# Performance work log

Measured on AMD Instinct MI355X. Metric: run time of the kernel, lower is better.

## Reference

```python
import jax, jax.numpy as jnp
import numpy as np

N, E = 20000, 320000
IN, HID, OUT, H = 128, 32, 1, 4
EPS = 1e-16  # PyG softmax epsilon


def _p(key, shape, scale=0.05):
    return jax.random.normal(key, shape, dtype=jnp.float32) * scale


def setup_inputs() -> dict:
    key = jax.random.key(0)
    ks = jax.random.split(key, 20)
    d = {
        "x": jax.random.normal(ks[0], (N, IN), dtype=jnp.float32),
        "edge_src": jax.random.randint(ks[1], (E,), 0, N, dtype=jnp.int32),
        "edge_dst": jax.random.randint(ks[2], (E,), 0, N, dtype=jnp.int32),
        # layer 1: TransformerConv(IN, HID, H)  ->  [N, H*HID]
        "W1q": _p(ks[3], (IN, H * HID)), "b1q": jnp.zeros((H * HID,), jnp.float32),
        "W1k": _p(ks[4], (IN, H * HID)), "b1k": jnp.zeros((H * HID,), jnp.float32),
        "W1v": _p(ks[5], (IN, H * HID)), "b1v": jnp.zeros((H * HID,), jnp.float32),
        "W1s": _p(ks[6], (IN, H * HID)), "b1s": jnp.zeros((H * HID,), jnp.float32),
        # layer 2: TransformerConv(H*HID, OUT, H) -> [N, H*OUT]
        "W2q": _p(ks[7], (H * HID, H * OUT)), "b2q": jnp.zeros((H * OUT,), jnp.float32),
        "W2k": _p(ks[8], (H * HID, H * OUT)), "b2k": jnp.zeros((H * OUT,), jnp.float32),
        "W2v": _p(ks[9], (H * HID, H * OUT)), "b2v": jnp.zeros((H * OUT,), jnp.float32),
        "W2s": _p(ks[10], (H * HID, H * OUT)), "b2s": jnp.zeros((H * OUT,), jnp.float32),
        # final nn.Linear(heads, 1)
        "Wl": _p(ks[11], (H, 1)), "bl": jnp.zeros((1,), jnp.float32),
    }
    return d


def transformer_conv(x, src, dst, Wq, bq, Wk, bk, Wv, bv, Ws, bs, heads, ch):
    n = x.shape[0]
    q = (x @ Wq + bq).reshape(n, heads, ch)
    k = (x @ Wk + bk).reshape(n, heads, ch)
    v = (x @ Wv + bv).reshape(n, heads, ch)
    qi, kj, vj = q[dst], k[src], v[src]            # [E,H,C] gathers
    score = (qi * kj).sum(-1) / jnp.sqrt(jnp.float32(ch))  # [E,H]
    m = jax.ops.segment_max(score, dst, num_segments=n)    # segment softmax by target
    e = jnp.exp(score - m[dst])
    s = jax.ops.segment_sum(e, dst, num_segments=n)
    alpha = e / (s[dst] + EPS)                              # [E,H]
    agg = jax.ops.segment_sum(alpha[:, :, None] * vj, dst, num_segments=n)  # [N,H,C]
    return agg.reshape(n, heads * ch) + x @ Ws + bs          # concat + root skip


def reference(x, edge_src, edge_dst,
              W1q, b1q, W1k, b1k, W1v, b1v, W1s, b1s,
              W2q, b2q, W2k, b2k, W2v, b2v, W2s, b2s,
              Wl, bl):
    h = transformer_conv(x, edge_src, edge_dst, W1q, b1q, W1k, b1k, W1v, b1v, W1s, b1s, H, HID)
    h = jax.nn.relu(h)  # dropout is identity in eval
    h = transformer_conv(h, edge_src, edge_dst, W2q, b2q, W2k, b2k, W2v, b2v, W2s, b2s, H, OUT)
    y = h @ Wl + bl                      # [N,1]
    return y.mean(axis=0, keepdims=True)  # [1,1]
```

## Files before the change

kernel.cpp:

```cpp
#include <hip/hip_runtime.h>
#include <math.h>

static constexpr float EPS_PYG = 1e-16f;
static constexpr float INV_SQRT32 = 0.17677669529663687f;

typedef short bf16x8 __attribute__((ext_vector_type(8)));
typedef float f32x4 __attribute__((ext_vector_type(4)));

__device__ inline unsigned short f2bf(float f) {
    union { float f; unsigned u; } x; x.f = f;
    unsigned r = x.u + 0x7FFFu + ((x.u >> 16) & 1u);
    return (unsigned short)(r >> 16);
}
__device__ inline float bf_hi(unsigned u) {
    union { unsigned u; float f; } x; x.u = u & 0xFFFF0000u; return x.f;
}
__device__ inline float bf_lo(unsigned u) {
    union { unsigned u; float f; } x; x.u = u << 16; return x.f;
}

__global__ void deg_kernel(const int* __restrict__ dst, int* __restrict__ deg, int E) {
    int e = blockIdx.x * blockDim.x + threadIdx.x;
    if (e < E) atomicAdd(&deg[dst[e]], 1);
}

__global__ __launch_bounds__(1024) void scan_kernel(const int* __restrict__ deg,
                                                    int* __restrict__ row_off, int n) {
    const int t = threadIdx.x;
    const int CH = (n + 1023) >> 10;
    const int base = t * CH;
    int vals[32];
    int sum = 0;
#pragma unroll 4
    for (int i = 0; i < CH; ++i) {
        int idx = base + i;
        int v = (idx < n) ? deg[idx] : 0;
        sum += v;
        vals[i] = sum;
    }
    const int lane = t & 63;
    const int wid = t >> 6;
    int wsum = sum;
#pragma unroll
    for (int off = 1; off < 64; off <<= 1) {
        int o = __shfl_up(wsum, off, 64);
        if (lane >= off) wsum += o;
    }
    __shared__ int wtot[16];
    if (lane == 63) wtot[wid] = wsum;
    __syncthreads();
    if (t < 64) {
        int v = (t < 16) ? wtot[t] : 0;
        int inc = v;
#pragma unroll
        for (int off = 1; off < 16; off <<= 1) {
            int o = __shfl_up(inc, off, 64);
            if (t >= off) inc += o;
        }
        if (t < 16) wtot[t] = inc - v;
    }
    __syncthreads();
    const int toff = wtot[wid] + (wsum - sum);
    if (t == 0) row_off[0] = 0;
#pragma unroll 4
    for (int i = 0; i < CH; ++i) {
        int idx = base + i;
        if (idx < n) row_off[idx + 1] = toff + vals[i];
    }
}

__global__ void scatter_kernel(const int* __restrict__ src, const int* __restrict__ dst,
                               const int* __restrict__ row_off, int* __restrict__ cursor,
                               int* __restrict__ csr_src, int E) {
    int e = blockIdx.x * blockDim.x + threadIdx.x;
    if (e < E) {
        int d = dst[e];
        int pos = row_off[d] + atomicAdd(&cursor[d], 1);
        csr_src[pos] = src[e];
    }
}

__global__ __launch_bounds__(256) void prep_kernel(
    const float4* __restrict__ X, ushort4* __restrict__ Xb, int total4,
    const float* __restrict__ Wq, const float* __restrict__ Wk,
    const float* __restrict__ Wv, const float* __restrict__ Wsk,
    unsigned short* __restrict__ Wbt)
{
    const int b = blockIdx.x;
    if (b < 4) {
        const float* W = (b == 0) ? Wq : (b == 1) ? Wk : (b == 2) ? Wv : Wsk;
        for (int i = threadIdx.x; i < 16384; i += 256) {
            int k = i >> 7, nn = i & 127;
            Wbt[b * 16384 + nn * 128 + k] = f2bf(W[i]);
        }
    } else {
        int i = (b - 4) * 256 + threadIdx.x;
        if (i < total4) {
            float4 v = X[i];
            ushort4 o;
            o.x = f2bf(v.x); o.y = f2bf(v.y); o.z = f2bf(v.z); o.w = f2bf(v.w);
            Xb[i] = o;
        }
    }
}

__global__ __launch_bounds__(256) void gemm1_mfma(
    const unsigned short* __restrict__ Xb, const unsigned short* __restrict__ Wbt,
    const float* __restrict__ bq, const float* __restrict__ bk,
    const float* __restrict__ bv, const float* __restrict__ bsk,
    float* __restrict__ Q, unsigned int* __restrict__ KV,
    float* __restrict__ S, int n)
{
    const int mat = blockIdx.y;
    const unsigned short* W = Wbt + (size_t)mat * 16384;
    const float* bias = (mat == 0) ? bq : (mat == 1) ? bk : (mat == 2) ? bv : bsk;

    const int tid  = threadIdx.x;
    const int wave = tid >> 6;
    const int lane = tid & 63;
    const int m    = lane & 15;
    const int quad = lane >> 4;
    const int r0   = blockIdx.x * 64 + wave * 16;

    int arow = r0 + m;
    if (arow >= n) arow = n - 1;

    f32x4 acc[8] = {};
#pragma unroll
    for (int kc = 0; kc < 128; kc += 32) {
        bf16x8 a = *(const bf16x8*)(Xb + (size_t)arow * 128 + kc + quad * 8);
#pragma unroll
        for (int ct = 0; ct < 8; ++ct) {
            bf16x8 bfr = *(const bf16x8*)(W + (ct * 16 + m) * 128 + kc + quad * 8);
            acc[ct] = __builtin_amdgcn_mfma_f32_16x16x32_bf16(a, bfr, acc[ct], 0, 0, 0);
        }
    }

#pragma unroll
    for (int ct = 0; ct < 8; ++ct) {
        const int col = ct * 16 + m;
        const float bb = bias[col];
#pragma unroll
        for (int r = 0; r < 4; ++r) {
            const int row = r0 + quad * 4 + r;
            if (row < n) {
                float val = acc[ct][r] + bb;
                size_t idx = (size_t)row * 128 + col;
                if (mat == 0)      Q[idx] = val;
                else if (mat == 3) S[idx] = val;
                else ((unsigned short*)KV)[idx * 2 + ((mat == 1) ? 1 : 0)] = f2bf(val);
            }
        }
    }
}

__global__ __launch_bounds__(128) void l1_agg_kernel(
    const float* __restrict__ Q, const unsigned int* __restrict__ KV,
    const float* __restrict__ S,
    const int* __restrict__ row_off, const int* __restrict__ csr_src,
    float* __restrict__ H1, int n)
{
    const int node = blockIdx.x;
    const int t = threadIdx.x;
    const float q = Q[(size_t)node * 128 + t];
    const int beg = row_off[node], end = row_off[node + 1];

    float l = 0.f, acc = 0.f;
    int pos = beg;
    for (; pos + 4 <= end; pos += 4) {
        int s0 = csr_src[pos];
        int s1 = csr_src[pos + 1];
        int s2 = csr_src[pos + 2];
        int s3 = csr_src[pos + 3];
        unsigned u0 = KV[(size_t)s0 * 128 + t];
        unsigned u1 = KV[(size_t)s1 * 128 + t];
        unsigned u2 = KV[(size_t)s2 * 128 + t];
        unsigned u3 = KV[(size_t)s3 * 128 + t];
        float p0 = q * bf_hi(u0), p1 = q * bf_hi(u1);
        float p2 = q * bf_hi(u2), p3 = q * bf_hi(u3);
        p0 += __shfl_xor(p0, 16, 32); p1 += __shfl_xor(p1, 16, 32);
        p2 += __shfl_xor(p2, 16, 32); p3 += __shfl_xor(p3, 16, 32);
        p0 += __shfl_xor(p0, 8, 32);  p1 += __shfl_xor(p1, 8, 32);
        p2 += __shfl_xor(p2, 8, 32);  p3 += __shfl_xor(p3, 8, 32);
        p0 += __shfl_xor(p0, 4, 32);  p1 += __shfl_xor(p1, 4, 32);
        p2 += __shfl_xor(p2, 4, 32);  p3 += __shfl_xor(p3, 4, 32);
        p0 += __shfl_xor(p0, 2, 32);  p1 += __shfl_xor(p1, 2, 32);
        p2 += __shfl_xor(p2, 2, 32);  p3 += __shfl_xor(p3, 2, 32);
        p0 += __shfl_xor(p0, 1, 32);  p1 += __shfl_xor(p1, 1, 32);
        p2 += __shfl_xor(p2, 1, 32);  p3 += __shfl_xor(p3, 1, 32);
        float e0 = __expf(p0 * INV_SQRT32);
        float e1 = __expf(p1 * INV_SQRT32);
        float e2 = __expf(p2 * INV_SQRT32);
        float e3 = __expf(p3 * INV_SQRT32);
        l   += (e0 + e1) + (e2 + e3);
        acc += (e0 * bf_lo(u0) + e1 * bf_lo(u1)) + (e2 * bf_lo(u2) + e3 * bf_lo(u3));
    }
    for (; pos < end; ++pos) {
        int s0 = csr_src[pos];
        unsigned u0 = KV[(size_t)s0 * 128 + t];
        float p0 = q * bf_hi(u0);
        p0 += __shfl_xor(p0, 16, 32);
        p0 += __shfl_xor(p0, 8, 32);
        p0 += __shfl_xor(p0, 4, 32);
        p0 += __shfl_xor(p0, 2, 32);
        p0 += __shfl_xor(p0, 1, 32);
        float e0 = __expf(p0 * INV_SQRT32);
        l += e0;
        acc += e0 * bf_lo(u0);
    }
    float out = acc / (l + EPS_PYG) + S[(size_t)node * 128 + t];
    H1[(size_t)node * 128 + t] = fmaxf(out, 0.f);
}

__global__ __launch_bounds__(256) void gemm2_kernel(
    const float* __restrict__ H1,
    const float* __restrict__ Wq, const float* __restrict__ Wk,
    const float* __restrict__ Wv, const float* __restrict__ Wsk,
    const float* __restrict__ bq, const float* __restrict__ bk,
    const float* __restrict__ bv, const float* __restrict__ bsk,
    float4* __restrict__ Q2, float4* __restrict__ K2,
    float4* __restrict__ V2, float4* __restrict__ S2, int n)
{
    __shared__ float Hs[64][129];
    __shared__ float Wt[128][16];
    __shared__ float bt[16];

    const int tid = threadIdx.x;
    const int r0 = blockIdx.x * 64;

    for (int i = tid; i < 2048; i += 256) {
        int row = i >> 4, col = i & 15;
        int mt = col >> 2, c = col & 3;
        const float* Wm = (mt == 0) ? Wq : (mt == 1) ? Wk : (mt == 2) ? Wv : Wsk;
        Wt[row][col] = Wm[row * 4 + c];
    }
    if (tid < 16) {
        int mt = tid >> 2;
        const float* bm = (mt == 0) ? bq : (mt == 1) ? bk : (mt == 2) ? bv : bsk;
        bt[tid] = bm[tid & 3];
    }
    for (int f = tid; f < 2048; f += 256) {
        int row = f >> 5, c4 = f & 31;
        float4 val = make_float4(0.f, 0.f, 0.f, 0.f);
        if (r0 + row < n) val = ((const float4*)H1)[(size_t)(r0 + row) * 32 + c4];
        Hs[row][c4 * 4 + 0] = val.x;
        Hs[row][c4 * 4 + 1] = val.y;
        Hs[row][c4 * 4 + 2] = val.z;
        Hs[row][c4 * 4 + 3] = val.w;
    }
    __syncthreads();

    const int nl = tid & 63;
    const int jg = tid >> 6;
    float a0 = 0.f, a1 = 0.f, a2 = 0.f, a3 = 0.f;
#pragma unroll 4
    for (int k = 0; k < 128; ++k) {
        float h = Hs[nl][k];
        a0 += h * Wt[k][jg * 4 + 0];
        a1 += h * Wt[k][jg * 4 + 1];
        a2 += h * Wt[k][jg * 4 + 2];
        a3 += h * Wt[k][jg * 4 + 3];
    }
    int node = r0 + nl;
    if (node < n) {
        float4 o = make_float4(a0 + bt[jg * 4 + 0], a1 + bt[jg * 4 + 1],
                               a2 + bt[jg * 4 + 2], a3 + bt[jg * 4 + 3]);
        float4* Cm = (jg == 0) ? Q2 : (jg == 1) ? K2 : (jg == 2) ? V2 : S2;
        Cm[node] = o;
    }
}

__global__ void init_out_kernel(float* __restrict__ out, const float* __restrict__ bl) {
    out[0] = bl[0];
}

__global__ __launch_bounds__(256) void l2_agg_kernel(
    const float4* __restrict__ Q2, const float4* __restrict__ K2,
    const float4* __restrict__ V2, const float4* __restrict__ S2,
    const int* __restrict__ row_off, const int* __restrict__ csr_src,
    const float* __restrict__ Wl, float* __restrict__ out, int n, float invn)
{
    const int nd = blockIdx.x * 256 + threadIdx.x;
    float y = 0.f;
    if (nd < n) {
        float4 q = Q2[nd];
        float l0 = 0.f, l1 = 0.f, l2 = 0.f, l3 = 0.f;
        float a0 = 0.f, a1 = 0.f, a2 = 0.f, a3 = 0.f;
        const int beg = row_off[nd], end = row_off[nd + 1];
        for (int pos = beg; pos < end; ++pos) {
            int src = csr_src[pos];
            float4 k = K2[src];
            float4 v = V2[src];
            float e0 = __expf(q.x * k.x);
            float e1 = __expf(q.y * k.y);
            float e2 = __expf(q.z * k.z);
            float e3 = __expf(q.w * k.w);
            l0 += e0; a0 += e0 * v.x;
            l1 += e1; a1 += e1 * v.y;
            l2 += e2; a2 += e2 * v.z;
            l3 += e3; a3 += e3 * v.w;
        }
        float4 sk = S2[nd];
        float h0 = a0 / (l0 + EPS_PYG) + sk.x;
        float h1 = a1 / (l1 + EPS_PYG) + sk.y;
        float h2 = a2 / (l2 + EPS_PYG) + sk.z;
        float h3 = a3 / (l3 + EPS_PYG) + sk.w;
        y = (h0 * Wl[0] + h1 * Wl[1] + h2 * Wl[2] + h3 * Wl[3]) * invn;
    }
    __shared__ float red[256];
    red[threadIdx.x] = y;
    __syncthreads();
    for (int off = 128; off > 0; off >>= 1) {
        if (threadIdx.x < (unsigned)off) red[threadIdx.x] += red[threadIdx.x + off];
        __syncthreads();
    }
    if (threadIdx.x == 0) atomicAdd(out, red[0]);
}

extern "C" void kernel_launch(void* const* d_in, const int* in_sizes, int n_in,
                              void* d_out, int out_size, void* d_ws, size_t ws_size,
                              hipStream_t stream) {
    const float* x        = (const float*)d_in[0];
    const int*   edge_src = (const int*)d_in[1];
    const int*   edge_dst = (const int*)d_in[2];
    const float* W1q = (const float*)d_in[3];  const float* b1q = (const float*)d_in[4];
    const float* W1k = (const float*)d_in[5];  const float* b1k = (const float*)d_in[6];
    const float* W1v = (const float*)d_in[7];  const float* b1v = (const float*)d_in[8];
    const float* W1s = (const float*)d_in[9];  const float* b1s = (const float*)d_in[10];
    const float* W2q = (const float*)d_in[11]; const float* b2q = (const float*)d_in[12];
    const float* W2k = (const float*)d_in[13]; const float* b2k = (const float*)d_in[14];
    const float* W2v = (const float*)d_in[15]; const float* b2v = (const float*)d_in[16];
    const float* W2s = (const float*)d_in[17]; const float* b2s = (const float*)d_in[18];
    const float* Wl  = (const float*)d_in[19]; const float* bl  = (const float*)d_in[20];

    const int N = in_sizes[0] / 128;
    const int E = in_sizes[1];
    float* out = (float*)d_out;

    float* ws  = (float*)d_ws;
    size_t off = 0;
    float*        Q1  = ws + off; off += (size_t)N * 128;
    unsigned int* KV  = (unsigned int*)(ws + off); off += (size_t)N * 128;
    float*        S1  = ws + off; off += (size_t)N * 128;
    float*        H1  = ws + off; off += (size_t)N * 128;
    float*        q2  = ws + off; off += (size_t)N * 4;
    float*        k2  = ws + off; off += (size_t)N * 4;
    float*        v2  = ws + off; off += (size_t)N * 4;
    float*        s2  = ws + off; off += (size_t)N * 4;
    unsigned short* Xb  = (unsigned short*)(ws + off); off += (size_t)N * 64;
    unsigned short* Wbt = (unsigned short*)(ws + off); off += 4 * 16384 / 2;
    int* ibase   = (int*)(ws + off);
    int* deg     = ibase;
    int* cursor  = ibase + N;
    int* row_off = ibase + 2 * N;
    int* csr_src = ibase + 3 * N + 1;

    hipMemsetAsync(deg, 0, (size_t)2 * N * sizeof(int), stream);
    deg_kernel<<<(E + 255) / 256, 256, 0, stream>>>(edge_dst, deg, E);
    scan_kernel<<<1, 1024, 0, stream>>>(deg, row_off, N);
    scatter_kernel<<<(E + 255) / 256, 256, 0, stream>>>(edge_src, edge_dst, row_off,
                                                        cursor, csr_src, E);

    const int total4 = N * 32;
    prep_kernel<<<4 + (total4 + 255) / 256, 256, 0, stream>>>(
        (const float4*)x, (ushort4*)Xb, total4, W1q, W1k, W1v, W1s, Wbt);

    {
        dim3 grid((N + 63) / 64, 4);
        gemm1_mfma<<<grid, 256, 0, stream>>>(Xb, Wbt, b1q, b1k, b1v, b1s,
                                             Q1, KV, S1, N);
    }
    l1_agg_kernel<<<N, 128, 0, stream>>>(Q1, KV, S1, row_off, csr_src, H1, N);

    gemm2_kernel<<<(N + 63) / 64, 256, 0, stream>>>(H1, W2q, W2k, W2v, W2s,
                                                    b2q, b2k, b2v, b2s,
                                                    (float4*)q2, (float4*)k2,
                                                    (float4*)v2, (float4*)s2, N);
    init_out_kernel<<<1, 1, 0, stream>>>(out, bl);
    l2_agg_kernel<<<(N + 255) / 256, 256, 0, stream>>>((const float4*)q2, (const float4*)k2,
                                                       (const float4*)v2, (const float4*)s2,
                                                       row_off, csr_src, Wl, out, N,
                                                       1.0f / (float)N);
}
```

Baseline: 258.1 us.

## Record atomic slots in degree pass, fuse K/V gemm, interleave layer-2 K/V

The degree pass now saves each edge's atomic slot, so the scatter pass computes its CSR position without a second atomic pass or a cursor memset. The layer-1 K and V projections are computed in the same block, sharing the A-operand loads and writing packed bf16 pairs as one 32-bit store instead of two strided half-word stores. Layer-2 K and V are interleaved so each edge gather reads adjacent data, and the out-init kernel is folded into the scan kernel. The cost is an extra E-sized slot buffer and more registers in the fused K/V gemm path.

```diff
diff --git a/kernel.cpp b/kernel.cpp
--- a/kernel.cpp
+++ b/kernel.cpp
@@ -19,13 +19,16 @@
     union { unsigned u; float f; } x; x.u = u << 16; return x.f;
 }
 
-__global__ void deg_kernel(const int* __restrict__ dst, int* __restrict__ deg, int E) {
+__global__ void deg_slot_kernel(const int* __restrict__ dst, int* __restrict__ deg,
+                                int* __restrict__ slot, int E) {
     int e = blockIdx.x * blockDim.x + threadIdx.x;
-    if (e < E) atomicAdd(&deg[dst[e]], 1);
+    if (e < E) slot[e] = atomicAdd(&deg[dst[e]], 1);
 }
 
 __global__ __launch_bounds__(1024) void scan_kernel(const int* __restrict__ deg,
-                                                    int* __restrict__ row_off, int n) {
+                                                    int* __restrict__ row_off, int n,
+                                                    float* __restrict__ out,
+                                                    const float* __restrict__ bl) {
     const int t = threadIdx.x;
     const int CH = (n + 1023) >> 10;
     const int base = t * CH;
@@ -61,7 +64,7 @@
     }
     __syncthreads();
     const int toff = wtot[wid] + (wsum - sum);
-    if (t == 0) row_off[0] = 0;
+    if (t == 0) { row_off[0] = 0; out[0] = bl[0]; }
 #pragma unroll 4
     for (int i = 0; i < CH; ++i) {
         int idx = base + i;
@@ -70,14 +73,10 @@
 }
 
 __global__ void scatter_kernel(const int* __restrict__ src, const int* __restrict__ dst,
-                               const int* __restrict__ row_off, int* __restrict__ cursor,
+                               const int* __restrict__ row_off, const int* __restrict__ slot,
                                int* __restrict__ csr_src, int E) {
     int e = blockIdx.x * blockDim.x + threadIdx.x;
-    if (e < E) {
-        int d = dst[e];
-        int pos = row_off[d] + atomicAdd(&cursor[d], 1);
-        csr_src[pos] = src[e];
-    }
+    if (e < E) csr_src[row_off[dst[e]] + slot[e]] = src[e];
 }
 
 __global__ __launch_bounds__(256) void prep_kernel(
@@ -111,9 +110,7 @@
     float* __restrict__ Q, unsigned int* __restrict__ KV,
     float* __restrict__ S, int n)
 {
-    const int mat = blockIdx.y;
-    const unsigned short* W = Wbt + (size_t)mat * 16384;
-    const float* bias = (mat == 0) ? bq : (mat == 1) ? bk : (mat == 2) ? bv : bsk;
+    const int mode = blockIdx.y;
 
     const int tid  = threadIdx.x;
     const int wave = tid >> 6;
@@ -125,30 +122,59 @@
     int arow = r0 + m;
     if (arow >= n) arow = n - 1;
 
-    f32x4 acc[8] = {};
-#pragma unroll
-    for (int kc = 0; kc < 128; kc += 32) {
-        bf16x8 a = *(const bf16x8*)(Xb + (size_t)arow * 128 + kc + quad * 8);
+    if (mode == 1) {
+        const unsigned short* WK = Wbt + 16384;
+        const unsigned short* WV = Wbt + 2 * 16384;
+        f32x4 accK[8] = {};
+        f32x4 accV[8] = {};
+#pragma unroll
+        for (int kc = 0; kc < 128; kc += 32) {
+            bf16x8 a = *(const bf16x8*)(Xb + (size_t)arow * 128 + kc + quad * 8);
+#pragma unroll
+            for (int ct = 0; ct < 8; ++ct) {
+                bf16x8 bk8 = *(const bf16x8*)(WK + (ct * 16 + m) * 128 + kc + quad * 8);
+                accK[ct] = __builtin_amdgcn_mfma_f32_16x16x32_bf16(a, bk8, accK[ct], 0, 0, 0);
+                bf16x8 bv8 = *(const bf16x8*)(WV + (ct * 16 + m) * 128 + kc + quad * 8);
+                accV[ct] = __builtin_amdgcn_mfma_f32_16x16x32_bf16(a, bv8, accV[ct], 0, 0, 0);
+            }
+        }
 #pragma unroll
         for (int ct = 0; ct < 8; ++ct) {
-            bf16x8 bfr = *(const bf16x8*)(W + (ct * 16 + m) * 128 + kc + quad * 8);
-            acc[ct] = __builtin_amdgcn_mfma_f32_16x16x32_bf16(a, bfr, acc[ct], 0, 0, 0);
-        }
-    }
-
-#pragma unroll
-    for (int ct = 0; ct < 8; ++ct) {
-        const int col = ct * 16 + m;
-        const float bb = bias[col];
-#pragma unroll
-        for (int r = 0; r < 4; ++r) {
-            const int row = r0 + quad * 4 + r;
-            if (row < n) {
-                float val = acc[ct][r] + bb;
-                size_t idx = (size_t)row * 128 + col;
-                if (mat == 0)      Q[idx] = val;
-                else if (mat == 3) S[idx] = val;
-                else ((unsigned short*)KV)[idx * 2 + ((mat == 1) ? 1 : 0)] = f2bf(val);
+            const int col = ct * 16 + m;
+            const float bbk = bk[col], bbv = bv[col];
+#pragma unroll
+            for (int r = 0; r < 4; ++r) {
+                const int row = r0 + quad * 4 + r;
+                if (row < n) {
+                    unsigned kb = f2bf(accK[ct][r] + bbk);
+                    unsigned vb = f2bf(accV[ct][r] + bbv);
+                    KV[(size_t)row * 128 + col] = (kb << 16) | vb;
+                }
+            }
+        }
+    } else {
+        const int mat = (mode == 0) ? 0 : 3;
+        const unsigned short* W = Wbt + (size_t)mat * 16384;
+        const float* bias = (mode == 0) ? bq : bsk;
+        float* C = (mode == 0) ? Q : S;
+        f32x4 acc[8] = {};
+#pragma unroll
+        for (int kc = 0; kc < 128; kc += 32) {
+            bf16x8 a = *(const bf16x8*)(Xb + (size_t)arow * 128 + kc + quad * 8);
+#pragma unroll
+            for (int ct = 0; ct < 8; ++ct) {
+                bf16x8 bfr = *(const bf16x8*)(W + (ct * 16 + m) * 128 + kc + quad * 8);
+                acc[ct] = __builtin_amdgcn_mfma_f32_16x16x32_bf16(a, bfr, acc[ct], 0, 0, 0);
+            }
+        }
+#pragma unroll
+        for (int ct = 0; ct < 8; ++ct) {
+            const int col = ct * 16 + m;
+            const float bb = bias[col];
+#pragma unroll
+            for (int r = 0; r < 4; ++r) {
+                const int row = r0 + quad * 4 + r;
+                if (row < n) C[(size_t)row * 128 + col] = acc[ct][r] + bb;
             }
         }
     }
@@ -218,8 +244,7 @@
     const float* __restrict__ Wv, const float* __restrict__ Wsk,
     const float* __restrict__ bq, const float* __restrict__ bk,
     const float* __restrict__ bv, const float* __restrict__ bsk,
-    float4* __restrict__ Q2, float4* __restrict__ K2,
-    float4* __restrict__ V2, float4* __restrict__ S2, int n)
+    float4* __restrict__ Q2, float4* __restrict__ KV2, float4* __restrict__ S2, int n)
 {
     __shared__ float Hs[64][129];
     __shared__ float Wt[128][16];
@@ -265,18 +290,16 @@
     if (node < n) {
         float4 o = make_float4(a0 + bt[jg * 4 + 0], a1 + bt[jg * 4 + 1],
                                a2 + bt[jg * 4 + 2], a3 + bt[jg * 4 + 3]);
-        float4* Cm = (jg == 0) ? Q2 : (jg == 1) ? K2 : (jg == 2) ? V2 : S2;
-        Cm[node] = o;
-    }
-}
-
-__global__ void init_out_kernel(float* __restrict__ out, const float* __restrict__ bl) {
-    out[0] = bl[0];
+        if (jg == 0)      Q2[node] = o;
+        else if (jg == 1) KV2[(size_t)node * 2 + 0] = o;
+        else if (jg == 2) KV2[(size_t)node * 2 + 1] = o;
+        else              S2[node] = o;
+    }
 }
 
 __global__ __launch_bounds__(256) void l2_agg_kernel(
-    const float4* __restrict__ Q2, const float4* __restrict__ K2,
-    const float4* __restrict__ V2, const float4* __restrict__ S2,
+    const float4* __restrict__ Q2, const float4* __restrict__ KV2,
+    const float4* __restrict__ S2,
     const int* __restrict__ row_off, const int* __restrict__ csr_src,
     const float* __restrict__ Wl, float* __restrict__ out, int n, float invn)
 {
@@ -289,8 +312,8 @@
         const int beg = row_off[nd], end = row_off[nd + 1];
         for (int pos = beg; pos < end; ++pos) {
             int src = csr_src[pos];
-            float4 k = K2[src];
-            float4 v = V2[src];
+            float4 k = KV2[(size_t)src * 2 + 0];
+            float4 v = KV2[(size_t)src * 2 + 1];
             float e0 = __expf(q.x * k.x);
             float e1 = __expf(q.y * k.y);
             float e2 = __expf(q.z * k.z);
@@ -344,29 +367,28 @@
     float*        S1  = ws + off; off += (size_t)N * 128;
     float*        H1  = ws + off; off += (size_t)N * 128;
     float*        q2  = ws + off; off += (size_t)N * 4;
-    float*        k2  = ws + off; off += (size_t)N * 4;
-    float*        v2  = ws + off; off += (size_t)N * 4;
+    float*        kv2 = ws + off; off += (size_t)N * 8;
     float*        s2  = ws + off; off += (size_t)N * 4;
     unsigned short* Xb  = (unsigned short*)(ws + off); off += (size_t)N * 64;
     unsigned short* Wbt = (unsigned short*)(ws + off); off += 4 * 16384 / 2;
     int* ibase   = (int*)(ws + off);
     int* deg     = ibase;
-    int* cursor  = ibase + N;
-    int* row_off = ibase + 2 * N;
-    int* csr_src = ibase + 3 * N + 1;
-
-    hipMemsetAsync(deg, 0, (size_t)2 * N * sizeof(int), stream);
-    deg_kernel<<<(E + 255) / 256, 256, 0, stream>>>(edge_dst, deg, E);
-    scan_kernel<<<1, 1024, 0, stream>>>(deg, row_off, N);
+    int* row_off = ibase + N;
+    int* slot    = ibase + 2 * N + 4;
+    int* csr_src = slot + E;
+
+    hipMemsetAsync(deg, 0, (size_t)N * sizeof(int), stream);
+    deg_slot_kernel<<<(E + 255) / 256, 256, 0, stream>>>(edge_dst, deg, slot, E);
+    scan_kernel<<<1, 1024, 0, stream>>>(deg, row_off, N, out, bl);
     scatter_kernel<<<(E + 255) / 256, 256, 0, stream>>>(edge_src, edge_dst, row_off,
-                                                        cursor, csr_src, E);
+                                                        slot, csr_src, E);
 
     const int total4 = N * 32;
     prep_kernel<<<4 + (total4 + 255) / 256, 256, 0, stream>>>(
         (const float4*)x, (ushort4*)Xb, total4, W1q, W1k, W1v, W1s, Wbt);
 
     {
-        dim3 grid((N + 63) / 64, 4);
+        dim3 grid((N + 63) / 64, 3);
         gemm1_mfma<<<grid, 256, 0, stream>>>(Xb, Wbt, b1q, b1k, b1v, b1s,
                                              Q1, KV, S1, N);
     }
@@ -374,11 +396,11 @@
 
     gemm2_kernel<<<(N + 63) / 64, 256, 0, stream>>>(H1, W2q, W2k, W2v, W2s,
                                                     b2q, b2k, b2v, b2s,
-                                                    (float4*)q2, (float4*)k2,
-                                                    (float4*)v2, (float4*)s2, N);
-    init_out_kernel<<<1, 1, 0, stream>>>(out, bl);
-    l2_agg_kernel<<<(N + 255) / 256, 256, 0, stream>>>((const float4*)q2, (const float4*)k2,
-                                                       (const float4*)v2, (const float4*)s2,
+                                                    (float4*)q2, (float4*)kv2,
+                                                    (float4*)s2, N);
+    l2_agg_kernel<<<(N + 255) / 256, 256, 0, stream>>>((const float4*)q2,
+                                                       (const float4*)kv2,
+                                                       (const float4*)s2,
                                                        row_off, csr_src, Wl, out, N,
                                                        1.0f / (float)N);
 }
```

Result: faster. 252.1 us (-2.3%).
